# Performance work log

Measured on AMD Instinct MI355X. Metric: run time of the kernel, lower is better.

Reference implementation:

```python
import jax, jax.numpy as jnp
import numpy as np

EPS = 1e-5


def _in_relu(y):
    # instance norm (no affine, biased var, eps=1e-5) + ReLU, y: [B,C,H,W]
    mu = jnp.mean(y, axis=(-2, -1), keepdims=True)
    var = jnp.mean((y - mu) ** 2, axis=(-2, -1), keepdims=True)
    return jax.nn.relu((y - mu) * jax.lax.rsqrt(var + EPS))


def _conv3(x, w, b):
    # x: [C,H,W], w: [O,I,3,3] -> [O,H,W]
    y = jax.lax.conv_general_dilated(x[None], w, (1, 1), ((1, 1), (1, 1)),
                                     dimension_numbers=('NCHW', 'OIHW', 'NCHW'))[0]
    return y + b[:, None, None]


def _mod_block(x, W, b, mod):
    # per-sample weight modulation: mod[n] * W, then conv+IN+relu; x: [B,C,H,W], mod: [B,O,I,3,3]
    y = jax.vmap(lambda xi, mi: _conv3(xi, mi * W, b))(x, mod)
    return _in_relu(y)


def _maxpool2(x):
    return jax.lax.reduce_window(x, -jnp.inf, jax.lax.max, (1, 1, 2, 2), (1, 1, 2, 2), 'VALID')


def _up2(x):
    B, C, H, W = x.shape
    # bilinear, half-pixel centers == PyTorch align_corners=False
    return jax.image.resize(x, (B, C, 2 * H, 2 * W), method='bilinear')


def _conv1x1(x, w, b):
    y = jax.lax.conv_general_dilated(x, w, (1, 1), 'VALID',
                                     dimension_numbers=('NCHW', 'OIHW', 'NCHW'))
    return y + b[None, :, None, None]


def setup_inputs() -> dict:
    key = jax.random.key(0)
    B, H, W = 8, 256, 256
    ks = iter(jax.random.split(key, 64))
    d = {}
    d['us_query_input'] = jax.random.normal(next(ks), (B, 1, H, W), jnp.float32)
    d['ksp_query_imgs'] = jax.random.normal(next(ks), (B, H, W, 2), jnp.float32)
    d['ksp_mask_query'] = jax.random.uniform(next(ks), (B, H, W), jnp.float32)
    down_io = [(1, 32), (32, 64), (64, 128), (128, 256)]
    up_io = [(512, 128), (256, 64), (128, 32), (64, 32)]
    for i, (ci, co) in enumerate(down_io):
        d[f'down_mod_{i}'] = jax.random.normal(next(ks), (B, co, ci, 3, 3), jnp.float32)
        d[f'W_d{i}'] = 0.05 * jax.random.normal(next(ks), (co, ci, 3, 3), jnp.float32)
        d[f'b_d{i}'] = 0.05 * jax.random.normal(next(ks), (co,), jnp.float32)
    d['latent_mod'] = jax.random.normal(next(ks), (B, 256, 256, 3, 3), jnp.float32)
    d['W_lat'] = 0.05 * jax.random.normal(next(ks), (256, 256, 3, 3), jnp.float32)
    d['b_lat'] = 0.05 * jax.random.normal(next(ks), (256,), jnp.float32)
    for i, (ci, co) in enumerate(up_io):
        d[f'up_mod_{i}'] = jax.random.normal(next(ks), (B, co, ci, 3, 3), jnp.float32)
        d[f'W_u{i}'] = 0.05 * jax.random.normal(next(ks), (co, ci, 3, 3), jnp.float32)
        d[f'b_u{i}'] = 0.05 * jax.random.normal(next(ks), (co,), jnp.float32)
    d['w_c1'] = 0.05 * jax.random.normal(next(ks), (16, 32, 1, 1), jnp.float32)
    d['b_c1'] = 0.05 * jax.random.normal(next(ks), (16,), jnp.float32)
    d['w_c2'] = 0.05 * jax.random.normal(next(ks), (1, 16, 1, 1), jnp.float32)
    d['b_c2'] = 0.05 * jax.random.normal(next(ks), (1,), jnp.float32)
    d['w_c3'] = 0.05 * jax.random.normal(next(ks), (1, 1, 1, 1), jnp.float32)
    d['b_c3'] = 0.05 * jax.random.normal(next(ks), (1,), jnp.float32)
    return d


def reference(us_query_input, ksp_query_imgs, ksp_mask_query,
              down_mod_0, down_mod_1, down_mod_2, down_mod_3,
              latent_mod, up_mod_0, up_mod_1, up_mod_2, up_mod_3,
              W_d0, b_d0, W_d1, b_d1, W_d2, b_d2, W_d3, b_d3,
              W_lat, b_lat,
              W_u0, b_u0, W_u1, b_u1, W_u2, b_u2, W_u3, b_u3,
              w_c1, b_c1, w_c2, b_c2, w_c3, b_c3):
    x0 = us_query_input
    out = x0
    skips = []
    downs = [(W_d0, b_d0, down_mod_0), (W_d1, b_d1, down_mod_1),
             (W_d2, b_d2, down_mod_2), (W_d3, b_d3, down_mod_3)]
    for Wc, bc, m in downs:
        out = _mod_block(out, Wc, bc, m)
        skips.append(out)
        out = _maxpool2(out)
    out = _mod_block(out, W_lat, b_lat, latent_mod)
    ups = [(W_u0, b_u0, up_mod_0), (W_u1, b_u1, up_mod_1),
           (W_u2, b_u2, up_mod_2), (W_u3, b_u3, up_mod_3)]
    for Wc, bc, m in ups:
        out = _up2(out)
        out = jnp.concatenate([out, skips.pop()], axis=1)
        out = _mod_block(out, Wc, bc, m)
    out = _conv1x1(_conv1x1(_conv1x1(out, w_c1, b_c1), w_c2, b_c2), w_c3, b_c3)
    out = out + x0
    # FFT data consistency
    pred = out[:, 0]                                  # [B,H,W]
    kpred = jnp.fft.fft2(pred, norm='ortho')
    ksp = ksp_query_imgs[..., 0] + 1j * ksp_query_imgs[..., 1]
    upd = ksp_mask_query * ksp + (1.0 - ksp_mask_query) * kpred
    img = jnp.fft.ifft2(upd, norm='ortho')
    return jnp.real(img)[:, None].astype(jnp.float32)   # [B,1,H,W]
```

## Files before the change

kernel.cpp:

```cpp
#include <hip/hip_runtime.h>


#define EPS_IN 1e-5f
constexpr int STST = 7936;

typedef __attribute__((ext_vector_type(8))) short short8;
typedef __attribute__((ext_vector_type(4))) short short4_t;
typedef __attribute__((ext_vector_type(4))) float f32x4;

__device__ __forceinline__ short f2bf(float f) {
    unsigned u = __float_as_uint(f);
    unsigned r = (u + 0x7fffu + ((u >> 16) & 1u)) >> 16;
    return (short)r;
}
__device__ __forceinline__ float bf2f(short s) {
    return __uint_as_float(((unsigned)(unsigned short)s) << 16);
}

struct SetupJobs {
    const float* W[8];
    const float* mod[8];
    short* wm[8];
    int Co[8];
    int Ci[8];
    int cum[9];
    const float *w1, *b1, *w2, *b2, *w3, *b3;
    float* eff;
    float* stats;
    int statN;
    int wmBlocks;
};

__global__ void setup_all(SetupJobs j)
{
    const int bx = blockIdx.x, tid = threadIdx.x;
    if (bx < j.wmBlocks) {
        int idx = bx * 256 + tid;
        if (idx >= j.cum[8]) return;
        int l = 0;
        while (idx >= j.cum[l + 1]) ++l;
        int local = idx - j.cum[l];
        const int Ci = j.Ci[l], Co = j.Co[l];
        int ci = local % Ci;
        int rem = local / Ci;
        int co = rem % Co;
        int b = rem / Co;
        const float* wp = j.W[l] + (size_t)(co * Ci + ci) * 9;
        const float* mp = j.mod[l] + ((size_t)((size_t)b * Co + co) * Ci + ci) * 9;
        short* wm = j.wm[l];
#pragma unroll
        for (int k = 0; k < 9; ++k)
            wm[(((size_t)(b * 9 + k) * Co + co) * Ci + ci)] = f2bf(wp[k] * mp[k]);
    } else if (bx == j.wmBlocks) {
        if (tid < 32) {
            float s = 0.f;
            for (int k = 0; k < 16; ++k) s += j.w2[k] * j.w1[k * 32 + tid];
            j.eff[tid] = j.w3[0] * s;
        }
        if (tid == 32) {
            float s = 0.f;
            for (int k = 0; k < 16; ++k) s += j.w2[k] * j.b1[k];
            j.eff[32] = j.w3[0] * (s + j.b2[0]) + j.b3[0];
        }
    } else {
        int i = (bx - j.wmBlocks - 1) * 256 + tid;
        if (i < j.statN) j.stats[i] = 0.f;
    }
}

template <int VR, int NCOG, bool UP>
__global__ __launch_bounds__(256) void conv3x3_cl(
    const short* __restrict__ x1, int Ci1,
    const short* __restrict__ x2,
    const float2* __restrict__ st1, float invHW1,
    const short* __restrict__ wm,
    short* __restrict__ y,
    float2* __restrict__ stats,
    int Ci, int Co, int H, int W)
{
    constexpr int TH = 4 * VR, SH = TH + 2, SW = 18;
    constexpr int STN = UP ? 128 : 1;
    constexpr int LH = UP ? (TH / 2 + 2) : 1;
    constexpr int LW = 10, LRW = LW * 8;
    constexpr bool DW = (TH * 16 * NCOG * 16) <= (SH * SW * 32);
    __shared__ __align__(16) short s_x[SH][SW][32];
    __shared__ float s_red[4][4][NCOG][4][2];
    __shared__ float2 s_st1[STN];
    __shared__ __align__(16) short s_lr[UP ? 4 : 1][LH][LRW];

    const int tid = threadIdx.x;
    const int lane = tid & 63, wv = tid >> 6;
    const int m = lane & 15, g = lane >> 4;

    const int b = blockIdx.x & 7;
    int r = blockIdx.x >> 3;
    const int nCoB = Co / (16 * NCOG);
    const int coblk = r % nCoB;
    const int tileId = r / nCoB;
    const int tilesx = W >> 4;
    const int tx0 = (tileId % tilesx) * 16;
    const int ty0 = (tileId / tilesx) * TH;
    const int co0 = coblk * (16 * NCOG);
    const int Ci2 = Ci - Ci1;
    const int Hs = H >> 1, Ws = W >> 1;
    const int bucket = tileId & 7;

    if (UP) {
        for (int i = tid; i < Ci1; i += 256) {
            float sx = 0.f, sy = 0.f;
#pragma unroll
            for (int k = 0; k < 8; ++k) {
                float2 v = st1[(size_t)k * STST + (size_t)b * Ci1 + i];
                sx += v.x; sy += v.y;
            }
            float mu = sx * invHW1;
            float var = sy * invHW1 - mu * mu;
            s_st1[i] = make_float2(mu, rsqrtf(var + EPS_IN));
        }
    }

    f32x4 acc[NCOG][VR];
#pragma unroll
    for (int cg = 0; cg < NCOG; ++cg)
#pragma unroll
        for (int rr = 0; rr < VR; ++rr) acc[cg][rr] = (f32x4)0.f;

    const short* wmb = wm + (size_t)b * 9 * Co * Ci;
    const short* x1b = x1 + (size_t)b * (UP ? (size_t)Hs * Ws : (size_t)H * W) * Ci1;
    const short* x2b = x2 + (size_t)b * H * W * Ci2;

    for (int ci0 = 0; ci0 < Ci; ci0 += 32) {
        __syncthreads();
        if (UP && ci0 < Ci1) {
            const int cb = ci0;
            const int ly0 = (ty0 >> 1) - 1, lx0 = (tx0 >> 1) - 1;
            for (int i2 = tid; i2 < 4 * LH * LW; i2 += 256) {
                int gg = i2 & 3, p2 = i2 >> 2;
                int jj = p2 / LW, ii = p2 - jj * LW;
                int sy2 = ly0 + jj; sy2 = sy2 < 0 ? 0 : (sy2 >= Hs ? Hs - 1 : sy2);
                int sx2 = lx0 + ii; sx2 = sx2 < 0 ? 0 : (sx2 >= Ws ? Ws - 1 : sx2);
                short8 v = *(const short8*)(x1b + ((size_t)sy2 * Ws + sx2) * Ci1 + cb + gg * 8);
                short8 o;
#pragma unroll
                for (int e = 0; e < 8; ++e) {
                    float2 sv = s_st1[cb + gg * 8 + e];
                    o[e] = f2bf(fmaxf(0.f, (bf2f(v[e]) - sv.x) * sv.y));
                }
                *(short8*)&s_lr[gg][jj][ii * 8] = o;
            }
            __syncthreads();
            for (int idx = tid; idx < SH * SW * 4; idx += 256) {
                int gg = idx & 3, pos = idx >> 2;
                int yy = pos / SW, xx = pos - yy * SW;
                int gy = ty0 + yy - 1, gx = tx0 + xx - 1;
                short8 v = (short8)0;
                if (gy >= 0 && gy < H && gx >= 0 && gx < W) {
                    int xk = gx >> 1, yk = gy >> 1;
                    int xo = gx & 1, yo = gy & 1;
                    int xa = xo ? xk : (xk > 0 ? xk - 1 : 0);
                    int xb = xo ? (xk + 1 < Ws ? xk + 1 : Ws - 1) : xk;
                    float wxa = xo ? 0.75f : 0.25f;
                    int ya = yo ? yk : (yk > 0 ? yk - 1 : 0);
                    int yb = yo ? (yk + 1 < Hs ? yk + 1 : Hs - 1) : yk;
                    float wya = yo ? 0.75f : 0.25f;
                    int ja = ya - ly0, jb = yb - ly0;
                    int ia = xa - lx0, ib2 = xb - lx0;
                    short8 vaa = *(const short8*)&s_lr[gg][ja][ia * 8];
                    short8 vab = *(const short8*)&s_lr[gg][ja][ib2 * 8];
                    short8 vba = *(const short8*)&s_lr[gg][jb][ia * 8];
                    short8 vbb = *(const short8*)&s_lr[gg][jb][ib2 * 8];
#pragma unroll
                    for (int e = 0; e < 8; ++e) {
                        float r0 = wxa * bf2f(vaa[e]) + (1.f - wxa) * bf2f(vab[e]);
                        float r1 = wxa * bf2f(vba[e]) + (1.f - wxa) * bf2f(vbb[e]);
                        v[e] = f2bf(wya * r0 + (1.f - wya) * r1);
                    }
                }
                *(short8*)&s_x[yy][xx][(gg ^ (xx & 3)) * 8] = v;
            }
        } else {
            const short* src; int C, cb;
            if (ci0 < Ci1) { src = x1b; C = Ci1; cb = ci0; }
            else           { src = x2b; C = Ci2; cb = ci0 - Ci1; }
            for (int idx = tid; idx < SH * SW * 4; idx += 256) {
                int gg = idx & 3, pos = idx >> 2;
                int yy = pos / SW, xx = pos - yy * SW;
                int gy = ty0 + yy - 1, gx = tx0 + xx - 1;
                short8 v = (short8)0;
                if (gy >= 0 && gy < H && gx >= 0 && gx < W)
                    v = *(const short8*)(src + ((size_t)gy * W + gx) * C + cb + gg * 8);
                *(short8*)&s_x[yy][xx][(gg ^ (xx & 3)) * 8] = v;
            }
        }
        __syncthreads();

        if constexpr (NCOG == 1) {
            short8 aT[9];
#pragma unroll
            for (int t = 0; t < 9; ++t)
                aT[t] = *(const short8*)(wmb + ((size_t)t * Co + co0 + m) * Ci + ci0 + g * 8);
#pragma unroll
            for (int t = 0; t < 9; ++t) {
                const int dy = t / 3, dx = t - 3 * (t / 3);
                const int xx = m + dx;
                const int sgo = (g ^ (xx & 3)) * 8;
#pragma unroll
                for (int rr = 0; rr < VR; ++rr) {
                    short8 bf = *(const short8*)&s_x[wv * VR + rr + dy][xx][sgo];
                    acc[0][rr] = __builtin_amdgcn_mfma_f32_16x16x32_bf16(aT[t], bf, acc[0][rr], 0, 0, 0);
                }
            }
        } else {
#pragma unroll
            for (int t = 0; t < 9; ++t) {
                const int dy = t / 3, dx = t - 3 * (t / 3);
                const short* wr = wmb + ((size_t)t * Co + co0) * Ci + ci0 + g * 8;
                short8 a[NCOG];
#pragma unroll
                for (int cg = 0; cg < NCOG; ++cg)
                    a[cg] = *(const short8*)(wr + (size_t)(cg * 16 + m) * Ci);
                const int xx = m + dx;
                const int sgo = (g ^ (xx & 3)) * 8;
#pragma unroll
                for (int rr = 0; rr < VR; ++rr) {
                    short8 bf = *(const short8*)&s_x[wv * VR + rr + dy][xx][sgo];
#pragma unroll
                    for (int cg = 0; cg < NCOG; ++cg)
                        acc[cg][rr] = __builtin_amdgcn_mfma_f32_16x16x32_bf16(a[cg], bf, acc[cg][rr], 0, 0, 0);
                }
            }
        }
    }

    if constexpr (DW) {
        __syncthreads();
        short* sd = (short*)&s_x[0][0][0];
#pragma unroll
        for (int cg = 0; cg < NCOG; ++cg)
#pragma unroll
            for (int rr = 0; rr < VR; ++rr) {
                short4_t o;
#pragma unroll
                for (int q = 0; q < 4; ++q) o[q] = f2bf(acc[cg][rr][q]);
                *(short4_t*)&sd[((wv * VR + rr) * 16 + m) * (NCOG * 16) + cg * 16 + g * 4] = o;
            }
        __syncthreads();
        constexpr int N16 = TH * 16 * NCOG * 2;
        constexpr int CPR = NCOG * 32;
        for (int c = tid; c < N16; c += 256) {
            int row = c / CPR;
            int o16 = c % CPR;
            int p = o16 / (NCOG * 2);
            int cw = o16 % (NCOG * 2);
            short8 v = *(short8*)&sd[(row * 16 + p) * (NCOG * 16) + cw * 8];
            *(short8*)(y + (((size_t)b * H + ty0 + row) * W + tx0 + p) * Co + co0 + cw * 8) = v;
        }
    } else {
        const int ox = tx0 + m;
#pragma unroll
        for (int cg = 0; cg < NCOG; ++cg)
#pragma unroll
            for (int rr = 0; rr < VR; ++rr) {
                int oy = ty0 + wv * VR + rr;
                short4_t o;
#pragma unroll
                for (int q = 0; q < 4; ++q) o[q] = f2bf(acc[cg][rr][q]);
                *(short4_t*)(y + (((size_t)b * H + oy) * W + ox) * Co + co0 + cg * 16 + g * 4) = o;
            }
    }

#pragma unroll
    for (int cg = 0; cg < NCOG; ++cg)
#pragma unroll
        for (int q = 0; q < 4; ++q) {
            float s = 0.f, s2 = 0.f;
#pragma unroll
            for (int rr = 0; rr < VR; ++rr) { float v = acc[cg][rr][q]; s += v; s2 += v * v; }
#pragma unroll
            for (int msk = 1; msk < 16; msk <<= 1) { s += __shfl_xor(s, msk); s2 += __shfl_xor(s2, msk); }
            if (m == 0) { s_red[wv][g][cg][q][0] = s; s_red[wv][g][cg][q][1] = s2; }
        }
    __syncthreads();
    for (int i = tid; i < 16 * NCOG; i += 256) {
        int q = i & 3, gg = (i >> 2) & 3, cg = i >> 4;
        float S = 0.f, S2 = 0.f;
#pragma unroll
        for (int w = 0; w < 4; ++w) { S += s_red[w][gg][cg][q][0]; S2 += s_red[w][gg][cg][q][1]; }
        float* sp = (float*)&stats[(size_t)bucket * STST + (size_t)b * Co + co0 + i];
        atomicAdd(sp, S); atomicAdd(sp + 1, S2);
    }
}

__global__ __launch_bounds__(256) void conv_d0_cl(
    const float* __restrict__ x0, const float* __restrict__ W,
    const float* __restrict__ mod, short* __restrict__ y,
    float2* __restrict__ stats)
{
    __shared__ float s[18][18];
    __shared__ float sw[32][9];
    __shared__ float s_red[8][32][2];
    __shared__ __align__(16) short sd[16][16][32];
    const int tid = threadIdx.x;
    const int tx = tid & 15, ty = tid >> 4;
    const int tx0 = (blockIdx.x & 15) * 16, ty0 = (blockIdx.x >> 4) * 16;
    const int b = blockIdx.y;
    if (tid < 288) sw[tid / 9][tid % 9] = W[tid] * mod[b * 288 + tid];
    for (int pos = tid; pos < 18 * 18; pos += 256) {
        int yy = pos / 18, xx = pos - yy * 18;
        int gy = ty0 + yy - 1, gx = tx0 + xx - 1;
        bool inb = gy >= 0 && gy < 256 && gx >= 0 && gx < 256;
        s[yy][xx] = inb ? x0[((size_t)b << 16) + gy * 256 + gx] : 0.f;
    }
    __syncthreads();
    float v[3][3];
#pragma unroll
    for (int r = 0; r < 3; ++r)
#pragma unroll
        for (int c = 0; c < 3; ++c) v[r][c] = s[ty + r][tx + c];
    float vals[32];
#pragma unroll
    for (int co = 0; co < 32; ++co) {
        float a = 0.f;
#pragma unroll
        for (int r = 0; r < 3; ++r)
#pragma unroll
            for (int c = 0; c < 3; ++c) a = fmaf(v[r][c], sw[co][r * 3 + c], a);
        vals[co] = a;
    }
#pragma unroll
    for (int j = 0; j < 4; ++j) {
        short8 o;
#pragma unroll
        for (int e = 0; e < 8; ++e) o[e] = f2bf(vals[j * 8 + e]);
        *(short8*)&sd[ty][tx][j * 8] = o;
    }
    __syncthreads();
    for (int c = tid; c < 1024; c += 256) {
        int row = c >> 6, o = c & 63;
        short8 vv = *(short8*)&sd[row][o >> 2][(o & 3) * 8];
        *(short8*)(y + (((size_t)b * 256 + ty0 + row) * 256 + tx0 + (o >> 2)) * 32 + (o & 3) * 8) = vv;
    }
    {
        const int c = tid & 31, grp = tid >> 5;
        const short* sdf = (const short*)sd;
        float ss = 0.f, ss2 = 0.f;
#pragma unroll
        for (int p = 0; p < 32; ++p) {
            float vv = bf2f(sdf[(grp * 32 + p) * 32 + c]);
            ss += vv; ss2 += vv * vv;
        }
        s_red[grp][c][0] = ss;
        s_red[grp][c][1] = ss2;
    }
    __syncthreads();
    if (tid < 32) {
        float S = 0.f, S2 = 0.f;
#pragma unroll
        for (int g2 = 0; g2 < 8; ++g2) { S += s_red[g2][tid][0]; S2 += s_red[g2][tid][1]; }
        int bucket = blockIdx.x & 7;
        float* sp = (float*)&stats[(size_t)bucket * STST + (size_t)b * 32 + tid];
        atomicAdd(sp, S); atomicAdd(sp + 1, S2);
    }
}

__global__ __launch_bounds__(256) void maxpool_cl(
    short* __restrict__ in, const float2* __restrict__ st, float invHW,
    short* __restrict__ out, int c8s, int ws, int hs, int total8)
{
    const int C = 8 << c8s;
    __shared__ float2 sst[2048];
    for (int i = threadIdx.x; i < 8 * C; i += 256) {
        int bb = i / C, c = i % C;
        float sx = 0.f, sy = 0.f;
#pragma unroll
        for (int k = 0; k < 8; ++k) {
            float2 v = st[(size_t)k * STST + (size_t)bb * C + c];
            sx += v.x; sy += v.y;
        }
        float mu = sx * invHW;
        sst[i] = make_float2(mu, rsqrtf(sy * invHW - mu * mu + EPS_IN));
    }
    __syncthreads();
    for (int idx = blockIdx.x * 256 + threadIdx.x; idx < total8; idx += gridDim.x * 256) {
        int c8 = idx & ((1 << c8s) - 1);
        int p = idx >> c8s;
        int x = p & ((1 << ws) - 1);
        int yy = (p >> ws) & ((1 << hs) - 1);
        int b = p >> (ws + hs);
        short* ip = in + (((size_t)b * (2 << hs) + 2 * yy) * (2 << ws) + 2 * x) * C + c8 * 8;
        size_t rs = (size_t)(2 << ws) * C;
        short8 v0 = *(const short8*)ip, v1 = *(const short8*)(ip + C);
        short8 v2 = *(const short8*)(ip + rs), v3 = *(const short8*)(ip + rs + C);
        short8 o, w0, w1, w2, w3;
#pragma unroll
        for (int e = 0; e < 8; ++e) {
            float2 sv = sst[b * C + c8 * 8 + e];
            float n0 = fmaxf(0.f, (bf2f(v0[e]) - sv.x) * sv.y);
            float n1 = fmaxf(0.f, (bf2f(v1[e]) - sv.x) * sv.y);
            float n2 = fmaxf(0.f, (bf2f(v2[e]) - sv.x) * sv.y);
            float n3 = fmaxf(0.f, (bf2f(v3[e]) - sv.x) * sv.y);
            w0[e] = f2bf(n0); w1[e] = f2bf(n1); w2[e] = f2bf(n2); w3[e] = f2bf(n3);
            o[e] = f2bf(fmaxf(fmaxf(n0, n1), fmaxf(n2, n3)));
        }
        *(short8*)ip = w0;
        *(short8*)(ip + C) = w1;
        *(short8*)(ip + rs) = w2;
        *(short8*)(ip + rs + C) = w3;
        *(short8*)(out + (size_t)idx * 8) = o;
    }
}

__global__ __launch_bounds__(256) void upsample_cl(
    const short* __restrict__ in, const float2* __restrict__ st, float invHW,
    short* __restrict__ out, int c8s, int wsi, int hsi, int total8)
{
    const int C = 8 << c8s;
    const int Win = 1 << wsi, Hin = 1 << hsi;
    __shared__ float2 sst[2048];
    for (int i = threadIdx.x; i < 8 * C; i += 256) {
        int bb = i / C, c = i % C;
        float sx = 0.f, sy = 0.f;
#pragma unroll
        for (int k = 0; k < 8; ++k) {
            float2 v = st[(size_t)k * STST + (size_t)bb * C + c];
            sx += v.x; sy += v.y;
        }
        float mu = sx * invHW;
        sst[i] = make_float2(mu, rsqrtf(sy * invHW - mu * mu + EPS_IN));
    }
    __syncthreads();
    for (int idx = blockIdx.x * 256 + threadIdx.x; idx < total8; idx += gridDim.x * 256) {
        int c8 = idx & ((1 << c8s) - 1);
        int p = idx >> c8s;
        int x = p & (2 * Win - 1);
        int yy = (p >> (wsi + 1)) & (2 * Hin - 1);
        int b = p >> (wsi + 1 + hsi + 1);
        int xk = x >> 1, yk = yy >> 1;
        int xa, xb; float wxa;
        if (x & 1) { xa = xk; xb = (xk + 1 < Win) ? xk + 1 : Win - 1; wxa = 0.75f; }
        else       { xa = (xk > 0) ? xk - 1 : 0; xb = xk; wxa = 0.25f; }
        int ya, yb; float wya;
        if (yy & 1) { ya = yk; yb = (yk + 1 < Hin) ? yk + 1 : Hin - 1; wya = 0.75f; }
        else        { ya = (yk > 0) ? yk - 1 : 0; yb = yk; wya = 0.25f; }
        const short* ib = in + (size_t)b * Hin * Win * C + c8 * 8;
        short8 vaa = *(const short8*)(ib + ((size_t)ya * Win + xa) * C);
        short8 vab = *(const short8*)(ib + ((size_t)ya * Win + xb) * C);
        short8 vba = *(const short8*)(ib + ((size_t)yb * Win + xa) * C);
        short8 vbb = *(const short8*)(ib + ((size_t)yb * Win + xb) * C);
        short8 o;
#pragma unroll
        for (int e = 0; e < 8; ++e) {
            float2 sv = sst[b * C + c8 * 8 + e];
            float aa = fmaxf(0.f, (bf2f(vaa[e]) - sv.x) * sv.y);
            float ab = fmaxf(0.f, (bf2f(vab[e]) - sv.x) * sv.y);
            float ba = fmaxf(0.f, (bf2f(vba[e]) - sv.x) * sv.y);
            float bb = fmaxf(0.f, (bf2f(vbb[e]) - sv.x) * sv.y);
            float r0 = wxa * aa + (1.f - wxa) * ab;
            float r1 = wxa * ba + (1.f - wxa) * bb;
            o[e] = f2bf(wya * r0 + (1.f - wya) * r1);
        }
        *(short8*)(out + (size_t)idx * 8) = o;
    }
}

template <bool INV>
__device__ __forceinline__ void fft256_tw(float2* s, const float2* tw, int tid)
{
    __syncthreads();
#pragma unroll
    for (int t = 0; t < 4; ++t) {
        int i = tid + t * 64;
        int r = __brev(i) >> 24;
        if (r > i) { float2 tmp = s[i]; s[i] = s[r]; s[r] = tmp; }
    }
    __syncthreads();
    for (int st = 1; st <= 8; ++st) {
        int half = 1 << (st - 1);
#pragma unroll
        for (int t = 0; t < 2; ++t) {
            int k = tid + t * 64;
            int gq = k >> (st - 1), j = k & (half - 1);
            int i0 = (gq << st) + j, i1 = i0 + half;
            float2 w = tw[j << (8 - st)];
            float cs = w.x, sn = INV ? -w.y : w.y;
            float2 a = s[i0], b = s[i1];
            float2 tt = make_float2(b.x * cs - b.y * sn, b.x * sn + b.y * cs);
            s[i0] = make_float2(a.x + tt.x, a.y + tt.y);
            s[i1] = make_float2(a.x - tt.x, a.y - tt.y);
        }
        __syncthreads();
    }
}

__device__ __forceinline__ void build_tw(float2* tw, int tid, int nthr)
{
    for (int i = tid; i < 128; i += nthr) {
        float ang = -6.283185307179586f * (float)i * (1.f / 256.f);
        float sn, cs;
        __sincosf(ang, &sn, &cs);
        tw[i] = make_float2(cs, sn);
    }
}

__global__ __launch_bounds__(64) void final_fft_rows(
    const short* __restrict__ act, const float2* __restrict__ st, float invHW,
    const float* __restrict__ x0, const float* __restrict__ eff,
    float2* __restrict__ cplx)
{
    __shared__ float2 s[256];
    __shared__ float2 s_tw[128];
    __shared__ float2 sst[32];
    __shared__ float seff[33];
    const int row = blockIdx.x, tid = threadIdx.x;
    const int b = row >> 8, yy = row & 255;
    build_tw(s_tw, tid, 64);
    if (tid < 32) {
        float sx = 0.f, sy = 0.f;
#pragma unroll
        for (int k = 0; k < 8; ++k) {
            float2 v = st[(size_t)k * STST + (size_t)b * 32 + tid];
            sx += v.x; sy += v.y;
        }
        float mu = sx * invHW;
        sst[tid] = make_float2(mu, rsqrtf(sy * invHW - mu * mu + EPS_IN));
    }
    if (tid < 33) seff[tid] = eff[tid];
    __syncthreads();
#pragma unroll
    for (int k = 0; k < 4; ++k) {
        int x = k * 64 + tid;
        const short8* a = (const short8*)(act + (((size_t)b * 256 + yy) * 256 + x) * 32);
        float sacc = seff[32] + x0[((size_t)b << 16) + (yy << 8) + x];
#pragma unroll
        for (int j = 0; j < 4; ++j) {
            short8 v = a[j];
#pragma unroll
            for (int e = 0; e < 8; ++e) {
                float2 sv = sst[j * 8 + e];
                sacc += seff[j * 8 + e] * fmaxf(0.f, (bf2f(v[e]) - sv.x) * sv.y);
            }
        }
        s[x] = make_float2(sacc, 0.f);
    }
    fft256_tw<false>(s, s_tw, tid);
    float2* o = cplx + (size_t)row * 256;
    for (int i = tid; i < 256; i += 64) o[i] = s[i];
}

__global__ __launch_bounds__(256) void fft_cols_combine8(
    float2* __restrict__ data, const float* __restrict__ ksp,
    const float* __restrict__ mask)
{
    __shared__ float2 s2[8][260];
    __shared__ float2 s_tw[128];
    const int tid = threadIdx.x;
    const int b = blockIdx.x >> 5;
    const int col0 = (blockIdx.x & 31) * 8;
    float2* base = data + (size_t)b * 65536 + col0;
    build_tw(s_tw, tid, 256);
    for (int idx = tid; idx < 2048; idx += 256) {
        int row = idx >> 3, c = idx & 7;
        s2[c][row] = base[row * 256 + c];
    }
    __syncthreads();
    const int c = tid >> 5, lt = tid & 31;
#pragma unroll
    for (int t = 0; t < 8; ++t) {
        int i = lt + t * 32;
        int r = __brev(i) >> 24;
        if (r > i) { float2 tmp = s2[c][i]; s2[c][i] = s2[c][r]; s2[c][r] = tmp; }
    }
    __syncthreads();
    for (int st = 1; st <= 8; ++st) {
        int half = 1 << (st - 1);
#pragma unroll
        for (int t = 0; t < 4; ++t) {
            int k = lt + t * 32;
            int gq = k >> (st - 1), j = k & (half - 1);
            int i0 = (gq << st) + j, i1 = i0 + half;
            float2 w = s_tw[j << (8 - st)];
            float cs = w.x, sn = w.y;
            float2 a = s2[c][i0], bb = s2[c][i1];
            float2 tt = make_float2(bb.x * cs - bb.y * sn, bb.x * sn + bb.y * cs);
            s2[c][i0] = make_float2(a.x + tt.x, a.y + tt.y);
            s2[c][i1] = make_float2(a.x - tt.x, a.y - tt.y);
        }
        __syncthreads();
    }
    for (int idx = tid; idx < 2048; idx += 256) {
        int row = idx >> 3, cc = idx & 7;
        size_t mi = ((size_t)b * 256 + row) * 256 + col0 + cc;
        float mval = mask[mi];
        float2 kp = s2[cc][row];
        float kr = ksp[mi * 2], ki = ksp[mi * 2 + 1];
        s2[cc][row] = make_float2(mval * kr + (1.f - mval) * kp.x * (1.f / 256.f),
                                  mval * ki + (1.f - mval) * kp.y * (1.f / 256.f));
    }
    __syncthreads();
#pragma unroll
    for (int t = 0; t < 8; ++t) {
        int i = lt + t * 32;
        int r = __brev(i) >> 24;
        if (r > i) { float2 tmp = s2[c][i]; s2[c][i] = s2[c][r]; s2[c][r] = tmp; }
    }
    __syncthreads();
    for (int st = 1; st <= 8; ++st) {
        int half = 1 << (st - 1);
#pragma unroll
        for (int t = 0; t < 4; ++t) {
            int k = lt + t * 32;
            int gq = k >> (st - 1), j = k & (half - 1);
            int i0 = (gq << st) + j, i1 = i0 + half;
            float2 w = s_tw[j << (8 - st)];
            float cs = w.x, sn = -w.y;
            float2 a = s2[c][i0], bb = s2[c][i1];
            float2 tt = make_float2(bb.x * cs - bb.y * sn, bb.x * sn + bb.y * cs);
            s2[c][i0] = make_float2(a.x + tt.x, a.y + tt.y);
            s2[c][i1] = make_float2(a.x - tt.x, a.y - tt.y);
        }
        __syncthreads();
    }
    for (int idx = tid; idx < 2048; idx += 256) {
        int row = idx >> 3, cc = idx & 7;
        base[row * 256 + cc] = s2[cc][row];
    }
}

__global__ __launch_bounds__(64) void fft_rows_inv(const float2* __restrict__ data,
                                                   float* __restrict__ out)
{
    __shared__ float2 s[256];
    __shared__ float2 s_tw[128];
    int row = blockIdx.x, tid = threadIdx.x;
    build_tw(s_tw, tid, 64);
    const float2* p = data + (size_t)row * 256;
    for (int i = tid; i < 256; i += 64) s[i] = p[i];
    fft256_tw<true>(s, s_tw, tid);
    float* o = out + (size_t)row * 256;
    for (int i = tid; i < 256; i += 64) o[i] = s[i].x * (1.f / 256.f);
}

extern "C" void kernel_launch(void* const* d_in, const int* in_sizes, int n_in,
                              void* d_out, int out_size, void* d_ws, size_t ws_size,
                              hipStream_t stream)
{
    (void)in_sizes; (void)n_in; (void)out_size; (void)ws_size;

    const float* x0 = (const float*)d_in[0];
    const float* ksp = (const float*)d_in[1];
    const float* mask = (const float*)d_in[2];
    const float* mod_d[4] = {(const float*)d_in[3], (const float*)d_in[6],
                             (const float*)d_in[9], (const float*)d_in[12]};
    const float* W_d[4] = {(const float*)d_in[4], (const float*)d_in[7],
                           (const float*)d_in[10], (const float*)d_in[13]};
    const float* mod_lat = (const float*)d_in[15];
    const float* W_lat = (const float*)d_in[16];
    const float* mod_u[4] = {(const float*)d_in[18], (const float*)d_in[21],
                             (const float*)d_in[24], (const float*)d_in[27]};
    const float* W_u[4] = {(const float*)d_in[19], (const float*)d_in[22],
                           (const float*)d_in[25], (const float*)d_in[28]};
    const float* w_c1 = (const float*)d_in[30];
    const float* b_c1 = (const float*)d_in[31];
    const float* w_c2 = (const float*)d_in[32];
    const float* b_c2 = (const float*)d_in[33];
    const float* w_c3 = (const float*)d_in[34];
    const float* b_c3 = (const float*)d_in[35];

    short* sA  = (short*)d_ws;
    short* sB  = sA + 16777216;
    short* sk0 = sB + 16777216;
    short* sk1 = sk0 + 16777216;
    short* sk2 = sk1 + 8388608;
    short* sk3 = sk2 + 4194304;
    short* wm_d1 = sk3 + 2097152;
    short* wm_d2 = wm_d1 + 147456;
    short* wm_d3 = wm_d2 + 589824;
    short* wm_lat = wm_d3 + 2359296;
    short* wm_u0 = wm_lat + 4718592;
    short* wm_u1 = wm_u0 + 4718592;
    short* wm_u2 = wm_u1 + 1179648;
    short* wm_u3 = wm_u2 + 294912;
    float2* cplx = (float2*)(wm_u3 + 147456);
    float2* stA = cplx + 524288;
    float* eff = (float*)(stA + 8 * STST);

    float2* st_d0 = stA + 0;
    float2* st_d1 = stA + 256;
    float2* st_d2 = stA + 768;
    float2* st_d3 = stA + 1792;
    float2* st_lat = stA + 3840;
    float2* st_u0 = stA + 5888;
    float2* st_u1 = stA + 6912;
    float2* st_u2 = stA + 7424;
    float2* st_u3 = stA + 7680;

    const float i64k = 1.f / 65536.f, i16k = 1.f / 16384.f, i4k = 1.f / 4096.f,
                i1k = 1.f / 1024.f, i256 = 1.f / 256.f;

    dim3 blk(256);

    SetupJobs jobs;
    const float* Wl[8]  = {W_d[1], W_d[2], W_d[3], W_lat, W_u[0], W_u[1], W_u[2], W_u[3]};
    const float* Ml[8]  = {mod_d[1], mod_d[2], mod_d[3], mod_lat, mod_u[0], mod_u[1], mod_u[2], mod_u[3]};
    short* WMl[8] = {wm_d1, wm_d2, wm_d3, wm_lat, wm_u0, wm_u1, wm_u2, wm_u3};
    int Col[8] = {64, 128, 256, 256, 128, 64, 32, 32};
    int Cil[8] = {32, 64, 128, 256, 512, 256, 128, 64};
    jobs.cum[0] = 0;
    for (int l = 0; l < 8; ++l) {
        jobs.W[l] = Wl[l]; jobs.mod[l] = Ml[l]; jobs.wm[l] = WMl[l];
        jobs.Co[l] = Col[l]; jobs.Ci[l] = Cil[l];
        jobs.cum[l + 1] = jobs.cum[l] + 8 * Col[l] * Cil[l];
    }
    jobs.w1 = w_c1; jobs.b1 = b_c1; jobs.w2 = w_c2; jobs.b2 = b_c2;
    jobs.w3 = w_c3; jobs.b3 = b_c3;
    jobs.eff = eff;
    jobs.stats = (float*)stA;
    jobs.statN = 8 * STST * 2;
    jobs.wmBlocks = (jobs.cum[8] + 255) / 256;
    int setupGrid = jobs.wmBlocks + 1 + (jobs.statN + 255) / 256;
    setup_all<<<setupGrid, blk, 0, stream>>>(jobs);

    conv_d0_cl<<<dim3(256, 8), blk, 0, stream>>>(x0, W_d[0], mod_d[0], sk0, st_d0);
    maxpool_cl<<<2048, blk, 0, stream>>>(sk0, st_d0, i64k, sA, 2, 7, 7, 524288);

    conv3x3_cl<4, 4, false><<<512, blk, 0, stream>>>(sA, 32, sA, stA, 0.f, wm_d1, sk1, st_d1, 32, 64, 128, 128);
    maxpool_cl<<<1024, blk, 0, stream>>>(sk1, st_d1, i16k, sA, 3, 6, 6, 262144);

    conv3x3_cl<2, 4, false><<<512, blk, 0, stream>>>(sA, 64, sA, stA, 0.f, wm_d2, sk2, st_d2, 64, 128, 64, 64);
    maxpool_cl<<<512, blk, 0, stream>>>(sk2, st_d2, i4k, sA, 4, 5, 5, 131072);

    conv3x3_cl<2, 2, false><<<512, blk, 0, stream>>>(sA, 128, sA, stA, 0.f, wm_d3, sk3, st_d3, 128, 256, 32, 32);
    maxpool_cl<<<256, blk, 0, stream>>>(sk3, st_d3, i1k, sA, 5, 4, 4, 65536);

    conv3x3_cl<2, 1, false><<<256, blk, 0, stream>>>(sA, 256, sA, stA, 0.f, wm_lat, sB, st_lat, 256, 256, 16, 16);

    upsample_cl<<<1024, blk, 0, stream>>>(sB, st_lat, i256, sA, 5, 4, 4, 262144);
    conv3x3_cl<2, 1, false><<<512, blk, 0, stream>>>(sA, 256, sk3, stA, 0.f, wm_u0, sB, st_u0, 512, 128, 32, 32);
    conv3x3_cl<2, 2, true><<<512, blk, 0, stream>>>(sB, 128, sk2, st_u0, i1k, wm_u1, sA, st_u1, 256, 64, 64, 64);
    conv3x3_cl<4, 2, true><<<512, blk, 0, stream>>>(sA, 64, sk1, st_u1, i4k, wm_u2, sB, st_u2, 128, 32, 128, 128);
    conv3x3_cl<4, 2, true><<<2048, blk, 0, stream>>>(sB, 32, sk0, st_u2, i16k, wm_u3, sA, st_u3, 64, 32, 256, 256);

    final_fft_rows<<<2048, 64, 0, stream>>>(sA, st_u3, i64k, x0, eff, cplx);

    fft_cols_combine8<<<256, blk, 0, stream>>>(cplx, ksp, mask);
    fft_rows_inv<<<2048, 64, 0, stream>>>(cplx, (float*)d_out);
}
```

Baseline: 441.7 us.

## Defer skip-tensor normalization into up-path conv loads; maxpool reads raw skips

```diff
diff --git a/kernel.cpp b/kernel.cpp
--- a/kernel.cpp
+++ b/kernel.cpp
@@ -68,11 +68,12 @@
     }
 }
 
-template <int VR, int NCOG, bool UP>
+template <int VR, int NCOG, bool UP, bool NRM2>
 __global__ __launch_bounds__(256) void conv3x3_cl(
     const short* __restrict__ x1, int Ci1,
     const short* __restrict__ x2,
     const float2* __restrict__ st1, float invHW1,
+    const float2* __restrict__ st2, float invHW2,
     const short* __restrict__ wm,
     short* __restrict__ y,
     float2* __restrict__ stats,
@@ -80,12 +81,14 @@
 {
     constexpr int TH = 4 * VR, SH = TH + 2, SW = 18;
     constexpr int STN = UP ? 128 : 1;
+    constexpr int ST2N = NRM2 ? 256 : 1;
     constexpr int LH = UP ? (TH / 2 + 2) : 1;
     constexpr int LW = 10, LRW = LW * 8;
     constexpr bool DW = (TH * 16 * NCOG * 16) <= (SH * SW * 32);
     __shared__ __align__(16) short s_x[SH][SW][32];
     __shared__ float s_red[4][4][NCOG][4][2];
     __shared__ float2 s_st1[STN];
+    __shared__ float2 s_st2[ST2N];
     __shared__ __align__(16) short s_lr[UP ? 4 : 1][LH][LRW];
 
     const int tid = threadIdx.x;
@@ -116,6 +119,19 @@
             float mu = sx * invHW1;
             float var = sy * invHW1 - mu * mu;
             s_st1[i] = make_float2(mu, rsqrtf(var + EPS_IN));
+        }
+    }
+    if (NRM2) {
+        for (int i = tid; i < Ci2; i += 256) {
+            float sx = 0.f, sy = 0.f;
+#pragma unroll
+            for (int k = 0; k < 8; ++k) {
+                float2 v = st2[(size_t)k * STST + (size_t)b * Ci2 + i];
+                sx += v.x; sy += v.y;
+            }
+            float mu = sx * invHW2;
+            float var = sy * invHW2 - mu * mu;
+            s_st2[i] = make_float2(mu, rsqrtf(var + EPS_IN));
         }
     }
 
@@ -182,13 +198,22 @@
             const short* src; int C, cb;
             if (ci0 < Ci1) { src = x1b; C = Ci1; cb = ci0; }
             else           { src = x2b; C = Ci2; cb = ci0 - Ci1; }
+            const bool nrm = NRM2 && (ci0 >= Ci1);
             for (int idx = tid; idx < SH * SW * 4; idx += 256) {
                 int gg = idx & 3, pos = idx >> 2;
                 int yy = pos / SW, xx = pos - yy * SW;
                 int gy = ty0 + yy - 1, gx = tx0 + xx - 1;
                 short8 v = (short8)0;
-                if (gy >= 0 && gy < H && gx >= 0 && gx < W)
+                if (gy >= 0 && gy < H && gx >= 0 && gx < W) {
                     v = *(const short8*)(src + ((size_t)gy * W + gx) * C + cb + gg * 8);
+                    if (nrm) {
+#pragma unroll
+                        for (int e = 0; e < 8; ++e) {
+                            float2 sv = s_st2[cb + gg * 8 + e];
+                            v[e] = f2bf(fmaxf(0.f, (bf2f(v[e]) - sv.x) * sv.y));
+                        }
+                    }
+                }
                 *(short8*)&s_x[yy][xx][(gg ^ (xx & 3)) * 8] = v;
             }
         }
@@ -364,7 +389,7 @@
 }
 
 __global__ __launch_bounds__(256) void maxpool_cl(
-    short* __restrict__ in, const float2* __restrict__ st, float invHW,
+    const short* __restrict__ in, const float2* __restrict__ st, float invHW,
     short* __restrict__ out, int c8s, int ws, int hs, int total8)
 {
     const int C = 8 << c8s;
@@ -387,25 +412,17 @@
         int x = p & ((1 << ws) - 1);
         int yy = (p >> ws) & ((1 << hs) - 1);
         int b = p >> (ws + hs);
-        short* ip = in + (((size_t)b * (2 << hs) + 2 * yy) * (2 << ws) + 2 * x) * C + c8 * 8;
+        const short* ip = in + (((size_t)b * (2 << hs) + 2 * yy) * (2 << ws) + 2 * x) * C + c8 * 8;
         size_t rs = (size_t)(2 << ws) * C;
         short8 v0 = *(const short8*)ip, v1 = *(const short8*)(ip + C);
         short8 v2 = *(const short8*)(ip + rs), v3 = *(const short8*)(ip + rs + C);
-        short8 o, w0, w1, w2, w3;
+        short8 o;
 #pragma unroll
         for (int e = 0; e < 8; ++e) {
             float2 sv = sst[b * C + c8 * 8 + e];
-            float n0 = fmaxf(0.f, (bf2f(v0[e]) - sv.x) * sv.y);
-            float n1 = fmaxf(0.f, (bf2f(v1[e]) - sv.x) * sv.y);
-            float n2 = fmaxf(0.f, (bf2f(v2[e]) - sv.x) * sv.y);
-            float n3 = fmaxf(0.f, (bf2f(v3[e]) - sv.x) * sv.y);
-            w0[e] = f2bf(n0); w1[e] = f2bf(n1); w2[e] = f2bf(n2); w3[e] = f2bf(n3);
-            o[e] = f2bf(fmaxf(fmaxf(n0, n1), fmaxf(n2, n3)));
-        }
-        *(short8*)ip = w0;
-        *(short8*)(ip + C) = w1;
-        *(short8*)(ip + rs) = w2;
-        *(short8*)(ip + rs + C) = w3;
+            float mx = fmaxf(fmaxf(bf2f(v0[e]), bf2f(v1[e])), fmaxf(bf2f(v2[e]), bf2f(v3[e])));
+            o[e] = f2bf(fmaxf(0.f, (mx - sv.x) * sv.y));
+        }
         *(short8*)(out + (size_t)idx * 8) = o;
     }
 }
@@ -723,22 +740,22 @@
     conv_d0_cl<<<dim3(256, 8), blk, 0, stream>>>(x0, W_d[0], mod_d[0], sk0, st_d0);
     maxpool_cl<<<2048, blk, 0, stream>>>(sk0, st_d0, i64k, sA, 2, 7, 7, 524288);
 
-    conv3x3_cl<4, 4, false><<<512, blk, 0, stream>>>(sA, 32, sA, stA, 0.f, wm_d1, sk1, st_d1, 32, 64, 128, 128);
+    conv3x3_cl<4, 4, false, false><<<512, blk, 0, stream>>>(sA, 32, sA, stA, 0.f, stA, 0.f, wm_d1, sk1, st_d1, 32, 64, 128, 128);
     maxpool_cl<<<1024, blk, 0, stream>>>(sk1, st_d1, i16k, sA, 3, 6, 6, 262144);
 
-    conv3x3_cl<2, 4, false><<<512, blk, 0, stream>>>(sA, 64, sA, stA, 0.f, wm_d2, sk2, st_d2, 64, 128, 64, 64);
+    conv3x3_cl<2, 4, false, false><<<512, blk, 0, stream>>>(sA, 64, sA, stA, 0.f, stA, 0.f, wm_d2, sk2, st_d2, 64, 128, 64, 64);
     maxpool_cl<<<512, blk, 0, stream>>>(sk2, st_d2, i4k, sA, 4, 5, 5, 131072);
 
-    conv3x3_cl<2, 2, false><<<512, blk, 0, stream>>>(sA, 128, sA, stA, 0.f, wm_d3, sk3, st_d3, 128, 256, 32, 32);
+    conv3x3_cl<2, 2, false, false><<<512, blk, 0, stream>>>(sA, 128, sA, stA, 0.f, stA, 0.f, wm_d3, sk3, st_d3, 128, 256, 32, 32);
     maxpool_cl<<<256, blk, 0, stream>>>(sk3, st_d3, i1k, sA, 5, 4, 4, 65536);
 
-    conv3x3_cl<2, 1, false><<<256, blk, 0, stream>>>(sA, 256, sA, stA, 0.f, wm_lat, sB, st_lat, 256, 256, 16, 16);
+    conv3x3_cl<2, 1, false, false><<<256, blk, 0, stream>>>(sA, 256, sA, stA, 0.f, stA, 0.f, wm_lat, sB, st_lat, 256, 256, 16, 16);
 
     upsample_cl<<<1024, blk, 0, stream>>>(sB, st_lat, i256, sA, 5, 4, 4, 262144);
-    conv3x3_cl<2, 1, false><<<512, blk, 0, stream>>>(sA, 256, sk3, stA, 0.f, wm_u0, sB, st_u0, 512, 128, 32, 32);
-    conv3x3_cl<2, 2, true><<<512, blk, 0, stream>>>(sB, 128, sk2, st_u0, i1k, wm_u1, sA, st_u1, 256, 64, 64, 64);
-    conv3x3_cl<4, 2, true><<<512, blk, 0, stream>>>(sA, 64, sk1, st_u1, i4k, wm_u2, sB, st_u2, 128, 32, 128, 128);
-    conv3x3_cl<4, 2, true><<<2048, blk, 0, stream>>>(sB, 32, sk0, st_u2, i16k, wm_u3, sA, st_u3, 64, 32, 256, 256);
+    conv3x3_cl<2, 1, false, true><<<512, blk, 0, stream>>>(sA, 256, sk3, stA, 0.f, st_d3, i1k, wm_u0, sB, st_u0, 512, 128, 32, 32);
+    conv3x3_cl<2, 2, true, true><<<512, blk, 0, stream>>>(sB, 128, sk2, st_u0, i1k, st_d2, i4k, wm_u1, sA, st_u1, 256, 64, 64, 64);
+    conv3x3_cl<4, 2, true, true><<<512, blk, 0, stream>>>(sA, 64, sk1, st_u1, i4k, st_d1, i16k, wm_u2, sB, st_u2, 128, 32, 128, 128);
+    conv3x3_cl<4, 2, true, true><<<2048, blk, 0, stream>>>(sB, 32, sk0, st_u2, i16k, st_d0, i64k, wm_u3, sA, st_u3, 64, 32, 256, 256);
 
     final_fft_rows<<<2048, 64, 0, stream>>>(sA, st_u3, i64k, x0, eff, cplx);
 
```

Result: slower. 462.5 us (+4.7%).
